# Kernel optimization log

Measured on AMD Instinct MI355X. Metric: run time of the kernel, lower is better.

Reference implementation:

```python
import jax, jax.numpy as jnp
import numpy as np

B, L, V, E, H = 64, 256, 256, 256, 1024

def setup_inputs() -> dict:
    key = jax.random.key(0)
    ks = jax.random.split(key, 7)
    inputs = jax.random.randint(ks[0], (B, L), 0, V, dtype=jnp.int32)
    embedding = jax.random.normal(ks[1], (V, E), dtype=jnp.float32)  # stddev=1.0 per emb_init
    # GRU weights: input projections (no bias) and hidden projections (with bias),
    # concatenated over gates [r, z, n].
    Wi = jax.random.normal(ks[2], (E, 3 * H), dtype=jnp.float32) / np.sqrt(E)
    Wh = jax.random.normal(ks[3], (H, 3 * H), dtype=jnp.float32) / np.sqrt(H)
    bh = jnp.zeros((3 * H,), dtype=jnp.float32)
    # Output dense (xavier_uniform-like scale)
    lim = np.sqrt(6.0 / (H + V))
    Wout = jax.random.uniform(ks[4], (H, V), dtype=jnp.float32, minval=-lim, maxval=lim)
    bout = jax.random.normal(ks[5], (V,), dtype=jnp.float32) * 1e-6
    return {"inputs": inputs, "embedding": embedding, "Wi": Wi, "Wh": Wh,
            "bh": bh, "Wout": Wout, "bout": bout}

def reference(inputs, embedding, Wi, Wh, bh, Wout, bout):
    # Embedding lookup: [B, L] -> [B, L, E]
    x = jnp.take(embedding, inputs, axis=0)
    # Precompute input-side gate projections for all timesteps (batched GEMM).
    xw = jnp.einsum('ble,ef->blf', x, Wi)  # [B, L, 3H]
    hidden = Wh.shape[0]

    def step(h, xw_t):
        gh = h @ Wh + bh                       # [B, 3H]
        xr, xz, xn = jnp.split(xw_t, 3, axis=-1)
        hr, hz, hn = jnp.split(gh, 3, axis=-1)
        r = jax.nn.sigmoid(xr + hr)
        z = jax.nn.sigmoid(xz + hz)
        n = jnp.tanh(xn + r * hn)
        h_new = (1.0 - z) * n + z * h          # GRUCell update
        return h_new, h_new

    h0 = jnp.zeros((x.shape[0], hidden), dtype=x.dtype)
    _, ys = jax.lax.scan(step, h0, jnp.swapaxes(xw, 0, 1))  # scan over time
    y = jnp.swapaxes(ys, 0, 1)                 # [B, L, H]
    logits = jnp.einsum('blh,hv->blv', y, Wout) + bout
    return logits
```

## Files before the change

kernel.cpp:

```cpp
#include <hip/hip_runtime.h>
#include <cstdint>
#include <math.h>

#define B_  64
#define L_  256
#define V_  256
#define E_  256
#define H_  1024
#define H3  3072

typedef __bf16 bf16x8 __attribute__((ext_vector_type(8)));
typedef float  f32x4  __attribute__((ext_vector_type(4)));

__device__ __forceinline__ unsigned short f2bf(float f) {
    union { float f; unsigned u; } v; v.f = f;
    unsigned r = v.u + 0x7fffu + ((v.u >> 16) & 1u);
    return (unsigned short)(r >> 16);
}

__device__ __forceinline__ int chunk_ok(bf16x8 v) {
    union { bf16x8 b; unsigned u[4]; } cv; cv.b = v;
    int ok = 1;
#pragma unroll
    for (int i = 0; i < 4; i++) {
        unsigned x = cv.u[i] ^ 0xAAAAAAAAu;
        ok &= (int)((x & 0xFFFFu) != 0u) & (int)((x >> 16) != 0u);
    }
    return ok;
}

__global__ __launch_bounds__(256) void prep_all(
        const float* __restrict__ Wh, const float* __restrict__ Wi,
        const float* __restrict__ Wout, const float* __restrict__ emb,
        unsigned short* __restrict__ WhT, unsigned short* __restrict__ WiT,
        unsigned short* __restrict__ WoutT, unsigned short* __restrict__ embB,
        unsigned short* __restrict__ h0b, uint4* __restrict__ poison) {
    __shared__ unsigned short tile[32][34];
    int bid = blockIdx.x;
    const float* src; unsigned short* dst; int rows, cols, nt, kt;
    if (bid < 3072)      { src = Wh;   dst = WhT;   rows = H_; cols = H3; nt = bid % 96; kt = bid / 96; }
    else if (bid < 3840) { int b = bid - 3072; src = Wi;   dst = WiT;   rows = E_; cols = H3; nt = b % 96; kt = b / 96; }
    else if (bid < 4096) { int b = bid - 3840; src = Wout; dst = WoutT; rows = H_; cols = V_; nt = b % 8;  kt = b / 8; }
    else if (bid < 4352) {
        int idx = (bid - 4096) * 256 + threadIdx.x;
        embB[idx] = f2bf(emb[idx]);
        h0b[idx]  = 0;
        return;
    } else {
        size_t T = (size_t)(bid - 4352) * 256 + threadIdx.x;
        uint4 v; v.x = v.y = v.z = v.w = 0xAAAAAAAAu;
        poison[T] = v;
        return;
    }
    int n0 = nt * 32, k0 = kt * 32;
    int tx = threadIdx.x & 31, ty = threadIdx.x >> 5;
#pragma unroll
    for (int j = 0; j < 32; j += 8)
        tile[tx][ty + j] = f2bf(src[(size_t)(k0 + ty + j) * cols + (n0 + tx)]);
    __syncthreads();
#pragma unroll
    for (int j = 0; j < 32; j += 8)
        dst[(size_t)(n0 + ty + j) * rows + (k0 + tx)] = tile[ty + j][tx];
}

__global__ __launch_bounds__(256, 1) void gru_persistent(
        unsigned short* __restrict__ hist,
        const unsigned short* __restrict__ WhT,
        const unsigned short* __restrict__ WiT,
        const unsigned short* __restrict__ embB,
        const int* __restrict__ tokens,
        const float* __restrict__ bh,
        unsigned short* __restrict__ yB) {
    __shared__ f32x4 red[2][4][6][64];

    int bid = blockIdx.x;
    int btile = bid & 3;
    int jtile = bid >> 2;
    int wave = threadIdx.x >> 6, lane = threadIdx.x & 63;
    int l16 = lane & 15, q = lane >> 4;
    int b0 = btile * 16, j0 = jtile * 16;
    int kbase = wave * 256;

    bf16x8 Wreg[3][8];
#pragma unroll
    for (int g = 0; g < 3; g++) {
        const bf16x8* Brow = (const bf16x8*)(WhT + (size_t)(g * H_ + j0 + l16) * H_);
#pragma unroll
        for (int kk = 0; kk < 8; kk++) {
            Wreg[g][kk] = Brow[(kbase >> 3) + kk * 4 + q];
            asm volatile("" : "+v"(Wreg[g][kk]));
        }
    }
    bf16x8 Wxreg[3][2];
#pragma unroll
    for (int g = 0; g < 3; g++) {
        const bf16x8* Bx = (const bf16x8*)(WiT + (size_t)(g * H_ + j0 + l16) * E_);
#pragma unroll
        for (int c = 0; c < 2; c++) {
            Wxreg[g][c] = Bx[wave * 8 + c * 4 + q];
            asm volatile("" : "+v"(Wxreg[g][c]));
        }
    }

    int Lp  = threadIdx.x & 63;
    int reg = threadIdx.x >> 6;
    int b_local = (Lp >> 4) * 4 + reg;
    int j_local = Lp & 15;
    int b = b0 + b_local, jg = j0 + j_local;
    float bhr = bh[jg];
    float bhz = bh[H_ + jg];
    float bhn = bh[2 * H_ + jg];
    asm volatile("" : "+v"(bhr), "+v"(bhz), "+v"(bhn));
    float hreg = 0.0f;

    const int tokrow = (b0 + l16) * L_;

    for (int t = 0; t < L_; t++) {
        const unsigned short* hist_t  = hist + (size_t)t * (B_ * H_);
        unsigned short*       hist_t1 = hist + (size_t)(t + 1) * (B_ * H_);

        int tok = tokens[tokrow + t];
        const bf16x8* Ax = (const bf16x8*)(embB + (size_t)tok * E_);
        bf16x8 ax0 = Ax[wave * 8 + q];
        bf16x8 ax1 = Ax[wave * 8 + 4 + q];
        f32x4 xacc[3] = {};
#pragma unroll
        for (int g = 0; g < 3; g++) {
            xacc[g] = __builtin_amdgcn_mfma_f32_16x16x32_bf16(ax0, Wxreg[g][0], xacc[g], 0, 0, 0);
            xacc[g] = __builtin_amdgcn_mfma_f32_16x16x32_bf16(ax1, Wxreg[g][1], xacc[g], 0, 0, 0);
        }

        const unsigned short* p = hist_t + (size_t)(b0 + l16) * H_ + kbase + q * 8;
        bf16x8 a0, a1, a2, a3, a4, a5, a6, a7;

        {
            int spins = 0;
            while (true) {
                asm volatile("global_load_dwordx4 %0, %1, off sc0 sc1" : "=v"(a0) : "v"(p));
                asm volatile("global_load_dwordx4 %0, %1, off sc0 sc1" : "=v"(a1) : "v"(p + 32));
                asm volatile("global_load_dwordx4 %0, %1, off sc0 sc1" : "=v"(a2) : "v"(p + 64));
                asm volatile("global_load_dwordx4 %0, %1, off sc0 sc1" : "=v"(a3) : "v"(p + 96));
                asm volatile("s_waitcnt vmcnt(0)"
                             : "+v"(a0), "+v"(a1), "+v"(a2), "+v"(a3) :: "memory");
                int ok = chunk_ok(a0) & chunk_ok(a1) & chunk_ok(a2) & chunk_ok(a3);
                if (__all(ok)) break;
                if (++spins > (1 << 18)) break;
                __builtin_amdgcn_s_sleep(1);
            }
        }
        asm volatile("global_load_dwordx4 %0, %1, off sc0 sc1" : "=v"(a4) : "v"(p + 128));
        asm volatile("global_load_dwordx4 %0, %1, off sc0 sc1" : "=v"(a5) : "v"(p + 160));
        asm volatile("global_load_dwordx4 %0, %1, off sc0 sc1" : "=v"(a6) : "v"(p + 192));
        asm volatile("global_load_dwordx4 %0, %1, off sc0 sc1" : "=v"(a7) : "v"(p + 224));

        f32x4 acc[3] = {};
#pragma unroll
        for (int g = 0; g < 3; g++) {
            acc[g] = __builtin_amdgcn_mfma_f32_16x16x32_bf16(a0, Wreg[g][0], acc[g], 0, 0, 0);
            acc[g] = __builtin_amdgcn_mfma_f32_16x16x32_bf16(a1, Wreg[g][1], acc[g], 0, 0, 0);
            acc[g] = __builtin_amdgcn_mfma_f32_16x16x32_bf16(a2, Wreg[g][2], acc[g], 0, 0, 0);
            acc[g] = __builtin_amdgcn_mfma_f32_16x16x32_bf16(a3, Wreg[g][3], acc[g], 0, 0, 0);
        }

        asm volatile("s_waitcnt vmcnt(0)"
                     : "+v"(a4), "+v"(a5), "+v"(a6), "+v"(a7) :: "memory");
        {
            int ok = chunk_ok(a4) & chunk_ok(a5) & chunk_ok(a6) & chunk_ok(a7);
            if (!__all(ok)) {
                int spins = 0;
                while (true) {
                    __builtin_amdgcn_s_sleep(1);
                    asm volatile("global_load_dwordx4 %0, %1, off sc0 sc1" : "=v"(a4) : "v"(p + 128));
                    asm volatile("global_load_dwordx4 %0, %1, off sc0 sc1" : "=v"(a5) : "v"(p + 160));
                    asm volatile("global_load_dwordx4 %0, %1, off sc0 sc1" : "=v"(a6) : "v"(p + 192));
                    asm volatile("global_load_dwordx4 %0, %1, off sc0 sc1" : "=v"(a7) : "v"(p + 224));
                    asm volatile("s_waitcnt vmcnt(0)"
                                 : "+v"(a4), "+v"(a5), "+v"(a6), "+v"(a7) :: "memory");
                    int ok2 = chunk_ok(a4) & chunk_ok(a5) & chunk_ok(a6) & chunk_ok(a7);
                    if (__all(ok2)) break;
                    if (++spins > (1 << 18)) break;
                }
            }
        }
#pragma unroll
        for (int g = 0; g < 3; g++) {
            acc[g] = __builtin_amdgcn_mfma_f32_16x16x32_bf16(a4, Wreg[g][4], acc[g], 0, 0, 0);
            acc[g] = __builtin_amdgcn_mfma_f32_16x16x32_bf16(a5, Wreg[g][5], acc[g], 0, 0, 0);
            acc[g] = __builtin_amdgcn_mfma_f32_16x16x32_bf16(a6, Wreg[g][6], acc[g], 0, 0, 0);
            acc[g] = __builtin_amdgcn_mfma_f32_16x16x32_bf16(a7, Wreg[g][7], acc[g], 0, 0, 0);
        }

        int par = t & 1;
#pragma unroll
        for (int g = 0; g < 3; g++) {
            red[par][wave][g][lane]     = acc[g];
            red[par][wave][3 + g][lane] = xacc[g];
        }
        __syncthreads();

        float gh0 = red[par][0][0][Lp][reg] + red[par][1][0][Lp][reg] + red[par][2][0][Lp][reg] + red[par][3][0][Lp][reg];
        float gh1 = red[par][0][1][Lp][reg] + red[par][1][1][Lp][reg] + red[par][2][1][Lp][reg] + red[par][3][1][Lp][reg];
        float gh2 = red[par][0][2][Lp][reg] + red[par][1][2][Lp][reg] + red[par][2][2][Lp][reg] + red[par][3][2][Lp][reg];
        float xr  = red[par][0][3][Lp][reg] + red[par][1][3][Lp][reg] + red[par][2][3][Lp][reg] + red[par][3][3][Lp][reg];
        float xz  = red[par][0][4][Lp][reg] + red[par][1][4][Lp][reg] + red[par][2][4][Lp][reg] + red[par][3][4][Lp][reg];
        float xn  = red[par][0][5][Lp][reg] + red[par][1][5][Lp][reg] + red[par][2][5][Lp][reg] + red[par][3][5][Lp][reg];

        float r = 1.0f / (1.0f + __expf(-(xr + gh0 + bhr)));
        float z = 1.0f / (1.0f + __expf(-(xz + gh1 + bhz)));
        float n = tanhf(xn + r * (gh2 + bhn));
        float hnew = (1.0f - z) * n + z * hreg;
        hreg = hnew;

        unsigned short hbv = f2bf(hnew);
        if (hbv == 0xAAAAu) hbv = 0xAAABu;

        {
            unsigned short* hp = hist_t1 + (size_t)b * H_ + jg;
            unsigned hv32 = hbv;
            asm volatile("global_store_short %0, %1, off sc0 sc1"
                         :: "v"(hp), "v"(hv32) : "memory");
        }
        yB[((size_t)b * L_ + t) * H_ + jg] = hbv;
    }
}

__global__ __launch_bounds__(256) void out_gemm(const unsigned short* __restrict__ yB,
                                                const unsigned short* __restrict__ WoutT,
                                                const float* __restrict__ bout,
                                                float* __restrict__ out) {
    int ntile = blockIdx.x;
    int mtile = blockIdx.y;
    int wave = threadIdx.x >> 6, lane = threadIdx.x & 63;
    int l16 = lane & 15, q = lane >> 4;

    int m = mtile * 64 + wave * 16 + l16;
    const bf16x8* Arow = (const bf16x8*)(yB + (size_t)m * H_);
    int n0 = ntile * 64;

    f32x4 acc[4] = {};
    for (int k0 = 0; k0 < H_; k0 += 32) {
        bf16x8 a = Arow[(k0 >> 3) + q];
#pragma unroll
        for (int j = 0; j < 4; j++) {
            const bf16x8* Brow = (const bf16x8*)(WoutT + (size_t)(n0 + j*16 + l16) * H_);
            bf16x8 b = Brow[(k0 >> 3) + q];
            acc[j] = __builtin_amdgcn_mfma_f32_16x16x32_bf16(a, b, acc[j], 0, 0, 0);
        }
    }
    int mrow = mtile * 64 + wave * 16 + q * 4;
#pragma unroll
    for (int j = 0; j < 4; j++) {
        int n = n0 + j * 16 + l16;
        float bias = bout[n];
#pragma unroll
        for (int r = 0; r < 4; r++)
            out[(size_t)(mrow + r) * V_ + n] = acc[j][r] + bias;
    }
}

extern "C" void kernel_launch(void* const* d_in, const int* in_sizes, int n_in,
                              void* d_out, int out_size, void* d_ws, size_t ws_size,
                              hipStream_t stream) {
    const int*   tokens = (const int*)  d_in[0];
    const float* emb    = (const float*)d_in[1];
    const float* Wi     = (const float*)d_in[2];
    const float* Wh     = (const float*)d_in[3];
    const float* bh     = (const float*)d_in[4];
    const float* Wout   = (const float*)d_in[5];
    const float* bout   = (const float*)d_in[6];
    float* out = (float*)d_out;

    char* ws = (char*)d_ws;
    size_t off = 0;
    auto alloc = [&](size_t bytes) -> void* {
        void* p = ws + off;
        off += (bytes + 255) & ~(size_t)255;
        return p;
    };
    unsigned short* WhT   = (unsigned short*)alloc((size_t)H3 * H_ * 2);
    unsigned short* WiT   = (unsigned short*)alloc((size_t)H3 * E_ * 2);
    unsigned short* WoutT = (unsigned short*)alloc((size_t)V_ * H_ * 2);
    unsigned short* embB  = (unsigned short*)alloc((size_t)V_ * E_ * 2);
    unsigned short* yB    = (unsigned short*)alloc((size_t)B_ * L_ * H_ * 2);
    unsigned short* hist  = (unsigned short*)alloc((size_t)(L_ + 1) * B_ * H_ * 2);

    prep_all<<<12544, 256, 0, stream>>>(Wh, Wi, Wout, emb, WhT, WiT, WoutT,
                                        embB, hist, (uint4*)(hist + (size_t)B_ * H_));

    {
        unsigned short* ah = hist;
        const unsigned short* aW = WhT; const unsigned short* aWx = WiT;
        const unsigned short* ae = embB; const int* at = tokens;
        const float* ab = bh; unsigned short* ay = yB;
        void* args[] = {&ah, &aW, &aWx, &ae, &at, &ab, &ay};
        hipError_t err = hipLaunchCooperativeKernel((void*)gru_persistent,
                                                    dim3(256), dim3(256), args, 0, stream);
        if (err != hipSuccess) {
            gru_persistent<<<dim3(256), dim3(256), 0, stream>>>(
                ah, aW, aWx, ae, at, ab, ay);
        }
    }

    out_gemm<<<dim3(4, 256), 256, 0, stream>>>(yB, WoutT, bout, out);
}
```

Baseline: 973.9 us.

## Give each GRU block two hidden tiles and relax coherent polling loads

Each persistent block now computes 32 hidden columns instead of 16, doubling the Wh/Wi weights held in registers. Only half of the launched blocks do work (g>=4 returns), so fewer blocks take part in each step's cross-block synchronisation. The polling loads of the previous hidden state start without the sc1 coherence bit and fall back to fully coherent loads with sleeps only after 512 spins. The gate nonlinearities switch to rcp-based sigmoid and tanh, and the LDS reduction layout is reorganised with an extra barrier. This risks register pressure from the doubled weight arrays and stale reads if the non-coherent polling misses fresh data.

```diff
diff --git a/kernel.cpp b/kernel.cpp
--- a/kernel.cpp
+++ b/kernel.cpp
@@ -27,6 +27,13 @@
         ok &= (int)((x & 0xFFFFu) != 0u) & (int)((x >> 16) != 0u);
     }
     return ok;
+}
+
+__device__ __forceinline__ float sigmoid_f(float x) {
+    return __builtin_amdgcn_rcpf(1.0f + __expf(-x));
+}
+__device__ __forceinline__ float tanh_f(float x) {
+    return 1.0f - 2.0f * __builtin_amdgcn_rcpf(1.0f + __expf(2.0f * x));
 }
 
 __global__ __launch_bounds__(256) void prep_all(
@@ -71,49 +78,61 @@
         const int* __restrict__ tokens,
         const float* __restrict__ bh,
         unsigned short* __restrict__ yB) {
-    __shared__ f32x4 red[2][4][6][64];
-
     int bid = blockIdx.x;
-    int btile = bid & 3;
-    int jtile = bid >> 2;
+    int g = bid & 7;
+    if (g >= 4) return;
+    int jpair = bid >> 3;
+    int b0 = g * 16;
+    int j0 = jpair * 32;
+
+    __shared__ float red[4][2][4][64][4];
+
     int wave = threadIdx.x >> 6, lane = threadIdx.x & 63;
     int l16 = lane & 15, q = lane >> 4;
-    int b0 = btile * 16, j0 = jtile * 16;
     int kbase = wave * 256;
 
-    bf16x8 Wreg[3][8];
-#pragma unroll
-    for (int g = 0; g < 3; g++) {
-        const bf16x8* Brow = (const bf16x8*)(WhT + (size_t)(g * H_ + j0 + l16) * H_);
-#pragma unroll
-        for (int kk = 0; kk < 8; kk++) {
-            Wreg[g][kk] = Brow[(kbase >> 3) + kk * 4 + q];
-            asm volatile("" : "+v"(Wreg[g][kk]));
-        }
-    }
-    bf16x8 Wxreg[3][2];
-#pragma unroll
-    for (int g = 0; g < 3; g++) {
-        const bf16x8* Bx = (const bf16x8*)(WiT + (size_t)(g * H_ + j0 + l16) * E_);
-#pragma unroll
-        for (int c = 0; c < 2; c++) {
-            Wxreg[g][c] = Bx[wave * 8 + c * 4 + q];
-            asm volatile("" : "+v"(Wxreg[g][c]));
-        }
-    }
-
-    int Lp  = threadIdx.x & 63;
-    int reg = threadIdx.x >> 6;
-    int b_local = (Lp >> 4) * 4 + reg;
-    int j_local = Lp & 15;
-    int b = b0 + b_local, jg = j0 + j_local;
-    float bhr = bh[jg];
-    float bhz = bh[H_ + jg];
-    float bhn = bh[2 * H_ + jg];
-    asm volatile("" : "+v"(bhr), "+v"(bhz), "+v"(bhn));
-    float hreg = 0.0f;
-
+    bf16x8 Wreg[2][3][8];
+#pragma unroll
+    for (int tl = 0; tl < 2; tl++) {
+#pragma unroll
+        for (int g3 = 0; g3 < 3; g3++) {
+            const bf16x8* Brow = (const bf16x8*)(WhT + (size_t)(g3 * H_ + j0 + tl * 16 + l16) * H_);
+#pragma unroll
+            for (int kk = 0; kk < 8; kk++) {
+                Wreg[tl][g3][kk] = Brow[(kbase >> 3) + kk * 4 + q];
+                asm volatile("" : "+v"(Wreg[tl][g3][kk]));
+            }
+        }
+    }
+    bf16x8 Wxreg[2][3][2];
+#pragma unroll
+    for (int tl = 0; tl < 2; tl++) {
+#pragma unroll
+        for (int g3 = 0; g3 < 3; g3++) {
+            const bf16x8* Bx = (const bf16x8*)(WiT + (size_t)(g3 * H_ + j0 + tl * 16 + l16) * E_);
+#pragma unroll
+            for (int c = 0; c < 2; c++) {
+                Wxreg[tl][g3][c] = Bx[wave * 8 + c * 4 + q];
+                asm volatile("" : "+v"(Wxreg[tl][g3][c]));
+            }
+        }
+    }
+
+    int j_local = lane & 15;
+    int b_local = (lane >> 4) * 4 + wave;
+    int b = b0 + b_local;
+    float bh_r[2], bh_z[2], bh_n[2];
+#pragma unroll
+    for (int tl = 0; tl < 2; tl++) {
+        int jg = j0 + tl * 16 + j_local;
+        bh_r[tl] = bh[jg];
+        bh_z[tl] = bh[H_ + jg];
+        bh_n[tl] = bh[2 * H_ + jg];
+        asm volatile("" : "+v"(bh_r[tl]), "+v"(bh_z[tl]), "+v"(bh_n[tl]));
+    }
+    float hreg[2] = {0.0f, 0.0f};
     const int tokrow = (b0 + l16) * L_;
+    int coh = 0;
 
     for (int t = 0; t < L_; t++) {
         const unsigned short* hist_t  = hist + (size_t)t * (B_ * H_);
@@ -123,11 +142,15 @@
         const bf16x8* Ax = (const bf16x8*)(embB + (size_t)tok * E_);
         bf16x8 ax0 = Ax[wave * 8 + q];
         bf16x8 ax1 = Ax[wave * 8 + 4 + q];
-        f32x4 xacc[3] = {};
-#pragma unroll
-        for (int g = 0; g < 3; g++) {
-            xacc[g] = __builtin_amdgcn_mfma_f32_16x16x32_bf16(ax0, Wxreg[g][0], xacc[g], 0, 0, 0);
-            xacc[g] = __builtin_amdgcn_mfma_f32_16x16x32_bf16(ax1, Wxreg[g][1], xacc[g], 0, 0, 0);
+        f32x4 accr[2] = {}, accz[2] = {}, acchn[2] = {}, accxn[2] = {};
+#pragma unroll
+        for (int tl = 0; tl < 2; tl++) {
+            accr[tl]  = __builtin_amdgcn_mfma_f32_16x16x32_bf16(ax0, Wxreg[tl][0][0], accr[tl], 0, 0, 0);
+            accr[tl]  = __builtin_amdgcn_mfma_f32_16x16x32_bf16(ax1, Wxreg[tl][0][1], accr[tl], 0, 0, 0);
+            accz[tl]  = __builtin_amdgcn_mfma_f32_16x16x32_bf16(ax0, Wxreg[tl][1][0], accz[tl], 0, 0, 0);
+            accz[tl]  = __builtin_amdgcn_mfma_f32_16x16x32_bf16(ax1, Wxreg[tl][1][1], accz[tl], 0, 0, 0);
+            accxn[tl] = __builtin_amdgcn_mfma_f32_16x16x32_bf16(ax0, Wxreg[tl][2][0], accxn[tl], 0, 0, 0);
+            accxn[tl] = __builtin_amdgcn_mfma_f32_16x16x32_bf16(ax1, Wxreg[tl][2][1], accxn[tl], 0, 0, 0);
         }
 
         const unsigned short* p = hist_t + (size_t)(b0 + l16) * H_ + kbase + q * 8;
@@ -136,30 +159,53 @@
         {
             int spins = 0;
             while (true) {
-                asm volatile("global_load_dwordx4 %0, %1, off sc0 sc1" : "=v"(a0) : "v"(p));
-                asm volatile("global_load_dwordx4 %0, %1, off sc0 sc1" : "=v"(a1) : "v"(p + 32));
-                asm volatile("global_load_dwordx4 %0, %1, off sc0 sc1" : "=v"(a2) : "v"(p + 64));
-                asm volatile("global_load_dwordx4 %0, %1, off sc0 sc1" : "=v"(a3) : "v"(p + 96));
+                if (coh) {
+                    asm volatile("global_load_dwordx4 %0, %1, off sc0 sc1" : "=v"(a0) : "v"(p));
+                    asm volatile("global_load_dwordx4 %0, %1, off sc0 sc1" : "=v"(a1) : "v"(p + 32));
+                    asm volatile("global_load_dwordx4 %0, %1, off sc0 sc1" : "=v"(a2) : "v"(p + 64));
+                    asm volatile("global_load_dwordx4 %0, %1, off sc0 sc1" : "=v"(a3) : "v"(p + 96));
+                } else {
+                    asm volatile("global_load_dwordx4 %0, %1, off sc0" : "=v"(a0) : "v"(p));
+                    asm volatile("global_load_dwordx4 %0, %1, off sc0" : "=v"(a1) : "v"(p + 32));
+                    asm volatile("global_load_dwordx4 %0, %1, off sc0" : "=v"(a2) : "v"(p + 64));
+                    asm volatile("global_load_dwordx4 %0, %1, off sc0" : "=v"(a3) : "v"(p + 96));
+                }
                 asm volatile("s_waitcnt vmcnt(0)"
                              : "+v"(a0), "+v"(a1), "+v"(a2), "+v"(a3) :: "memory");
                 int ok = chunk_ok(a0) & chunk_ok(a1) & chunk_ok(a2) & chunk_ok(a3);
                 if (__all(ok)) break;
-                if (++spins > (1 << 18)) break;
-                __builtin_amdgcn_s_sleep(1);
-            }
-        }
-        asm volatile("global_load_dwordx4 %0, %1, off sc0 sc1" : "=v"(a4) : "v"(p + 128));
-        asm volatile("global_load_dwordx4 %0, %1, off sc0 sc1" : "=v"(a5) : "v"(p + 160));
-        asm volatile("global_load_dwordx4 %0, %1, off sc0 sc1" : "=v"(a6) : "v"(p + 192));
-        asm volatile("global_load_dwordx4 %0, %1, off sc0 sc1" : "=v"(a7) : "v"(p + 224));
-
-        f32x4 acc[3] = {};
-#pragma unroll
-        for (int g = 0; g < 3; g++) {
-            acc[g] = __builtin_amdgcn_mfma_f32_16x16x32_bf16(a0, Wreg[g][0], acc[g], 0, 0, 0);
-            acc[g] = __builtin_amdgcn_mfma_f32_16x16x32_bf16(a1, Wreg[g][1], acc[g], 0, 0, 0);
-            acc[g] = __builtin_amdgcn_mfma_f32_16x16x32_bf16(a2, Wreg[g][2], acc[g], 0, 0, 0);
-            acc[g] = __builtin_amdgcn_mfma_f32_16x16x32_bf16(a3, Wreg[g][3], acc[g], 0, 0, 0);
+                ++spins;
+                if (spins == 512) coh = 1;
+                if (spins > (1 << 18)) break;
+                if (coh) __builtin_amdgcn_s_sleep(1);
+            }
+        }
+        if (coh) {
+            asm volatile("global_load_dwordx4 %0, %1, off sc0 sc1" : "=v"(a4) : "v"(p + 128));
+            asm volatile("global_load_dwordx4 %0, %1, off sc0 sc1" : "=v"(a5) : "v"(p + 160));
+            asm volatile("global_load_dwordx4 %0, %1, off sc0 sc1" : "=v"(a6) : "v"(p + 192));
+            asm volatile("global_load_dwordx4 %0, %1, off sc0 sc1" : "=v"(a7) : "v"(p + 224));
+        } else {
+            asm volatile("global_load_dwordx4 %0, %1, off sc0" : "=v"(a4) : "v"(p + 128));
+            asm volatile("global_load_dwordx4 %0, %1, off sc0" : "=v"(a5) : "v"(p + 160));
+            asm volatile("global_load_dwordx4 %0, %1, off sc0" : "=v"(a6) : "v"(p + 192));
+            asm volatile("global_load_dwordx4 %0, %1, off sc0" : "=v"(a7) : "v"(p + 224));
+        }
+
+#pragma unroll
+        for (int tl = 0; tl < 2; tl++) {
+            accr[tl]  = __builtin_amdgcn_mfma_f32_16x16x32_bf16(a0, Wreg[tl][0][0], accr[tl], 0, 0, 0);
+            accr[tl]  = __builtin_amdgcn_mfma_f32_16x16x32_bf16(a1, Wreg[tl][0][1], accr[tl], 0, 0, 0);
+            accr[tl]  = __builtin_amdgcn_mfma_f32_16x16x32_bf16(a2, Wreg[tl][0][2], accr[tl], 0, 0, 0);
+            accr[tl]  = __builtin_amdgcn_mfma_f32_16x16x32_bf16(a3, Wreg[tl][0][3], accr[tl], 0, 0, 0);
+            accz[tl]  = __builtin_amdgcn_mfma_f32_16x16x32_bf16(a0, Wreg[tl][1][0], accz[tl], 0, 0, 0);
+            accz[tl]  = __builtin_amdgcn_mfma_f32_16x16x32_bf16(a1, Wreg[tl][1][1], accz[tl], 0, 0, 0);
+            accz[tl]  = __builtin_amdgcn_mfma_f32_16x16x32_bf16(a2, Wreg[tl][1][2], accz[tl], 0, 0, 0);
+            accz[tl]  = __builtin_amdgcn_mfma_f32_16x16x32_bf16(a3, Wreg[tl][1][3], accz[tl], 0, 0, 0);
+            acchn[tl] = __builtin_amdgcn_mfma_f32_16x16x32_bf16(a0, Wreg[tl][2][0], acchn[tl], 0, 0, 0);
+            acchn[tl] = __builtin_amdgcn_mfma_f32_16x16x32_bf16(a1, Wreg[tl][2][1], acchn[tl], 0, 0, 0);
+            acchn[tl] = __builtin_amdgcn_mfma_f32_16x16x32_bf16(a2, Wreg[tl][2][2], acchn[tl], 0, 0, 0);
+            acchn[tl] = __builtin_amdgcn_mfma_f32_16x16x32_bf16(a3, Wreg[tl][2][3], acchn[tl], 0, 0, 0);
         }
 
         asm volatile("s_waitcnt vmcnt(0)"
@@ -169,58 +215,82 @@
             if (!__all(ok)) {
                 int spins = 0;
                 while (true) {
-                    __builtin_amdgcn_s_sleep(1);
-                    asm volatile("global_load_dwordx4 %0, %1, off sc0 sc1" : "=v"(a4) : "v"(p + 128));
-                    asm volatile("global_load_dwordx4 %0, %1, off sc0 sc1" : "=v"(a5) : "v"(p + 160));
-                    asm volatile("global_load_dwordx4 %0, %1, off sc0 sc1" : "=v"(a6) : "v"(p + 192));
-                    asm volatile("global_load_dwordx4 %0, %1, off sc0 sc1" : "=v"(a7) : "v"(p + 224));
+                    if (coh) {
+                        asm volatile("global_load_dwordx4 %0, %1, off sc0 sc1" : "=v"(a4) : "v"(p + 128));
+                        asm volatile("global_load_dwordx4 %0, %1, off sc0 sc1" : "=v"(a5) : "v"(p + 160));
+                        asm volatile("global_load_dwordx4 %0, %1, off sc0 sc1" : "=v"(a6) : "v"(p + 192));
+                        asm volatile("global_load_dwordx4 %0, %1, off sc0 sc1" : "=v"(a7) : "v"(p + 224));
+                    } else {
+                        asm volatile("global_load_dwordx4 %0, %1, off sc0" : "=v"(a4) : "v"(p + 128));
+                        asm volatile("global_load_dwordx4 %0, %1, off sc0" : "=v"(a5) : "v"(p + 160));
+                        asm volatile("global_load_dwordx4 %0, %1, off sc0" : "=v"(a6) : "v"(p + 192));
+                        asm volatile("global_load_dwordx4 %0, %1, off sc0" : "=v"(a7) : "v"(p + 224));
+                    }
                     asm volatile("s_waitcnt vmcnt(0)"
                                  : "+v"(a4), "+v"(a5), "+v"(a6), "+v"(a7) :: "memory");
                     int ok2 = chunk_ok(a4) & chunk_ok(a5) & chunk_ok(a6) & chunk_ok(a7);
                     if (__all(ok2)) break;
-                    if (++spins > (1 << 18)) break;
+                    ++spins;
+                    if (spins == 512) coh = 1;
+                    if (spins > (1 << 18)) break;
+                    if (coh) __builtin_amdgcn_s_sleep(1);
                 }
             }
         }
 #pragma unroll
-        for (int g = 0; g < 3; g++) {
-            acc[g] = __builtin_amdgcn_mfma_f32_16x16x32_bf16(a4, Wreg[g][4], acc[g], 0, 0, 0);
-            acc[g] = __builtin_amdgcn_mfma_f32_16x16x32_bf16(a5, Wreg[g][5], acc[g], 0, 0, 0);
-            acc[g] = __builtin_amdgcn_mfma_f32_16x16x32_bf16(a6, Wreg[g][6], acc[g], 0, 0, 0);
-            acc[g] = __builtin_amdgcn_mfma_f32_16x16x32_bf16(a7, Wreg[g][7], acc[g], 0, 0, 0);
-        }
-
-        int par = t & 1;
-#pragma unroll
-        for (int g = 0; g < 3; g++) {
-            red[par][wave][g][lane]     = acc[g];
-            red[par][wave][3 + g][lane] = xacc[g];
-        }
+        for (int tl = 0; tl < 2; tl++) {
+            accr[tl]  = __builtin_amdgcn_mfma_f32_16x16x32_bf16(a4, Wreg[tl][0][4], accr[tl], 0, 0, 0);
+            accr[tl]  = __builtin_amdgcn_mfma_f32_16x16x32_bf16(a5, Wreg[tl][0][5], accr[tl], 0, 0, 0);
+            accr[tl]  = __builtin_amdgcn_mfma_f32_16x16x32_bf16(a6, Wreg[tl][0][6], accr[tl], 0, 0, 0);
+            accr[tl]  = __builtin_amdgcn_mfma_f32_16x16x32_bf16(a7, Wreg[tl][0][7], accr[tl], 0, 0, 0);
+            accz[tl]  = __builtin_amdgcn_mfma_f32_16x16x32_bf16(a4, Wreg[tl][1][4], accz[tl], 0, 0, 0);
+            accz[tl]  = __builtin_amdgcn_mfma_f32_16x16x32_bf16(a5, Wreg[tl][1][5], accz[tl], 0, 0, 0);
+            accz[tl]  = __builtin_amdgcn_mfma_f32_16x16x32_bf16(a6, Wreg[tl][1][6], accz[tl], 0, 0, 0);
+            accz[tl]  = __builtin_amdgcn_mfma_f32_16x16x32_bf16(a7, Wreg[tl][1][7], accz[tl], 0, 0, 0);
+            acchn[tl] = __builtin_amdgcn_mfma_f32_16x16x32_bf16(a4, Wreg[tl][2][4], acchn[tl], 0, 0, 0);
+            acchn[tl] = __builtin_amdgcn_mfma_f32_16x16x32_bf16(a5, Wreg[tl][2][5], acchn[tl], 0, 0, 0);
+            acchn[tl] = __builtin_amdgcn_mfma_f32_16x16x32_bf16(a6, Wreg[tl][2][6], acchn[tl], 0, 0, 0);
+            acchn[tl] = __builtin_amdgcn_mfma_f32_16x16x32_bf16(a7, Wreg[tl][2][7], acchn[tl], 0, 0, 0);
+        }
+
         __syncthreads();
-
-        float gh0 = red[par][0][0][Lp][reg] + red[par][1][0][Lp][reg] + red[par][2][0][Lp][reg] + red[par][3][0][Lp][reg];
-        float gh1 = red[par][0][1][Lp][reg] + red[par][1][1][Lp][reg] + red[par][2][1][Lp][reg] + red[par][3][1][Lp][reg];
-        float gh2 = red[par][0][2][Lp][reg] + red[par][1][2][Lp][reg] + red[par][2][2][Lp][reg] + red[par][3][2][Lp][reg];
-        float xr  = red[par][0][3][Lp][reg] + red[par][1][3][Lp][reg] + red[par][2][3][Lp][reg] + red[par][3][3][Lp][reg];
-        float xz  = red[par][0][4][Lp][reg] + red[par][1][4][Lp][reg] + red[par][2][4][Lp][reg] + red[par][3][4][Lp][reg];
-        float xn  = red[par][0][5][Lp][reg] + red[par][1][5][Lp][reg] + red[par][2][5][Lp][reg] + red[par][3][5][Lp][reg];
-
-        float r = 1.0f / (1.0f + __expf(-(xr + gh0 + bhr)));
-        float z = 1.0f / (1.0f + __expf(-(xz + gh1 + bhz)));
-        float n = tanhf(xn + r * (gh2 + bhn));
-        float hnew = (1.0f - z) * n + z * hreg;
-        hreg = hnew;
-
-        unsigned short hbv = f2bf(hnew);
-        if (hbv == 0xAAAAu) hbv = 0xAAABu;
-
-        {
+#pragma unroll
+        for (int tl = 0; tl < 2; tl++) {
+            *(f32x4*)&red[wave][tl][0][lane][0] = accr[tl];
+            *(f32x4*)&red[wave][tl][1][lane][0] = accz[tl];
+            *(f32x4*)&red[wave][tl][2][lane][0] = acchn[tl];
+            *(f32x4*)&red[wave][tl][3][lane][0] = accxn[tl];
+        }
+        __syncthreads();
+
+#pragma unroll
+        for (int tl = 0; tl < 2; tl++) {
+            float s0 = 0.f, s1 = 0.f, s2 = 0.f, s3 = 0.f;
+#pragma unroll
+            for (int w = 0; w < 4; w++) {
+                s0 += red[w][tl][0][lane][wave];
+                s1 += red[w][tl][1][lane][wave];
+                s2 += red[w][tl][2][lane][wave];
+                s3 += red[w][tl][3][lane][wave];
+            }
+            float r = sigmoid_f(s0 + bh_r[tl]);
+            float z = sigmoid_f(s1 + bh_z[tl]);
+            float n = tanh_f(s3 + r * (s2 + bh_n[tl]));
+            float hnew = (1.0f - z) * n + z * hreg[tl];
+            hreg[tl] = hnew;
+
+            unsigned short hbv = f2bf(hnew);
+            if (hbv == 0xAAAAu) hbv = 0xAAABu;
+
+            int jg = j0 + tl * 16 + j_local;
             unsigned short* hp = hist_t1 + (size_t)b * H_ + jg;
             unsigned hv32 = hbv;
             asm volatile("global_store_short %0, %1, off sc0 sc1"
                          :: "v"(hp), "v"(hv32) : "memory");
-        }
-        yB[((size_t)b * L_ + t) * H_ + jg] = hbv;
+            asm volatile("global_store_short %0, %1, off"
+                         :: "v"(hp), "v"(hv32) : "memory");
+            yB[((size_t)b * L_ + t) * H_ + jg] = hbv;
+        }
     }
 }
 
```

Result: slower. 1.529 ms (+57.0%).

## Coalesce GRU hidden-state stores via LDS and single-pass poll on all chunks

Applied to the files above, without the earlier changes.

Each block now stages its 16x16 new hidden-state tile in shared memory. A few lanes then write it as 16-byte stores to both the history buffer and yB, replacing many 2-byte stores. The readiness poll issues all eight chunk loads up front and waits once. Because chunks are now written atomically in 16-byte units, it checks only the head word of each chunk, and it sleeps only after 16 spins. The next timestep's token and embedding row are prefetched during the current step. In exchange there is an extra block barrier per step, and correctness depends on the 16-byte stores being seen whole.

```diff
diff --git a/kernel.cpp b/kernel.cpp
--- a/kernel.cpp
+++ b/kernel.cpp
@@ -11,6 +11,7 @@
 
 typedef __bf16 bf16x8 __attribute__((ext_vector_type(8)));
 typedef float  f32x4  __attribute__((ext_vector_type(4)));
+typedef unsigned u32x4 __attribute__((ext_vector_type(4)));
 
 __device__ __forceinline__ unsigned short f2bf(float f) {
     union { float f; unsigned u; } v; v.f = f;
@@ -18,15 +19,10 @@
     return (unsigned short)(r >> 16);
 }
 
-__device__ __forceinline__ int chunk_ok(bf16x8 v) {
+__device__ __forceinline__ int head_ok(bf16x8 v) {
     union { bf16x8 b; unsigned u[4]; } cv; cv.b = v;
-    int ok = 1;
-#pragma unroll
-    for (int i = 0; i < 4; i++) {
-        unsigned x = cv.u[i] ^ 0xAAAAAAAAu;
-        ok &= (int)((x & 0xFFFFu) != 0u) & (int)((x >> 16) != 0u);
-    }
-    return ok;
+    unsigned x = cv.u[0];
+    return (int)((x & 0xFFFFu) != 0xAAAAu) & (int)((x >> 16) != 0xAAAAu);
 }
 
 __global__ __launch_bounds__(256) void prep_all(
@@ -72,6 +68,7 @@
         const float* __restrict__ bh,
         unsigned short* __restrict__ yB) {
     __shared__ f32x4 red[2][4][6][64];
+    __shared__ unsigned short htile[16][24];
 
     int bid = blockIdx.x;
     int btile = bid & 3;
@@ -106,52 +103,74 @@
     int reg = threadIdx.x >> 6;
     int b_local = (Lp >> 4) * 4 + reg;
     int j_local = Lp & 15;
-    int b = b0 + b_local, jg = j0 + j_local;
-    float bhr = bh[jg];
-    float bhz = bh[H_ + jg];
-    float bhn = bh[2 * H_ + jg];
+    float bhr = bh[j0 + j_local];
+    float bhz = bh[H_ + j0 + j_local];
+    float bhn = bh[2 * H_ + j0 + j_local];
     asm volatile("" : "+v"(bhr), "+v"(bhz), "+v"(bhn));
     float hreg = 0.0f;
 
     const int tokrow = (b0 + l16) * L_;
+    int srow  = wave * 4 + ((lane >> 1) & 3);
+    int shalf = lane & 1;
+
+    int tok = tokens[tokrow];
+    const bf16x8* Ax0p = (const bf16x8*)(embB + (size_t)tok * E_);
+    bf16x8 ax0 = Ax0p[wave * 8 + q];
+    bf16x8 ax1 = Ax0p[wave * 8 + 4 + q];
 
     for (int t = 0; t < L_; t++) {
         const unsigned short* hist_t  = hist + (size_t)t * (B_ * H_);
         unsigned short*       hist_t1 = hist + (size_t)(t + 1) * (B_ * H_);
-
-        int tok = tokens[tokrow + t];
-        const bf16x8* Ax = (const bf16x8*)(embB + (size_t)tok * E_);
-        bf16x8 ax0 = Ax[wave * 8 + q];
-        bf16x8 ax1 = Ax[wave * 8 + 4 + q];
+        const unsigned short* p = hist_t + (size_t)(b0 + l16) * H_ + kbase + q * 8;
+
+        bf16x8 a0, a1, a2, a3, a4, a5, a6, a7;
+        asm volatile("global_load_dwordx4 %0, %1, off sc0 sc1" : "=v"(a0) : "v"(p));
+        asm volatile("global_load_dwordx4 %0, %1, off sc0 sc1" : "=v"(a1) : "v"(p + 32));
+        asm volatile("global_load_dwordx4 %0, %1, off sc0 sc1" : "=v"(a2) : "v"(p + 64));
+        asm volatile("global_load_dwordx4 %0, %1, off sc0 sc1" : "=v"(a3) : "v"(p + 96));
+        asm volatile("global_load_dwordx4 %0, %1, off sc0 sc1" : "=v"(a4) : "v"(p + 128));
+        asm volatile("global_load_dwordx4 %0, %1, off sc0 sc1" : "=v"(a5) : "v"(p + 160));
+        asm volatile("global_load_dwordx4 %0, %1, off sc0 sc1" : "=v"(a6) : "v"(p + 192));
+        asm volatile("global_load_dwordx4 %0, %1, off sc0 sc1" : "=v"(a7) : "v"(p + 224));
+
         f32x4 xacc[3] = {};
 #pragma unroll
         for (int g = 0; g < 3; g++) {
             xacc[g] = __builtin_amdgcn_mfma_f32_16x16x32_bf16(ax0, Wxreg[g][0], xacc[g], 0, 0, 0);
             xacc[g] = __builtin_amdgcn_mfma_f32_16x16x32_bf16(ax1, Wxreg[g][1], xacc[g], 0, 0, 0);
         }
-
-        const unsigned short* p = hist_t + (size_t)(b0 + l16) * H_ + kbase + q * 8;
-        bf16x8 a0, a1, a2, a3, a4, a5, a6, a7;
+        int tnext = (t + 1 < L_) ? (t + 1) : (L_ - 1);
+        const int* tp = tokens + tokrow + tnext;
+        int tok_next;
+        asm volatile("global_load_dword %0, %1, off" : "=v"(tok_next) : "v"(tp));
 
         {
             int spins = 0;
             while (true) {
+                asm volatile("s_waitcnt vmcnt(0)"
+                             : "+v"(a0), "+v"(a1), "+v"(a2), "+v"(a3),
+                               "+v"(a4), "+v"(a5), "+v"(a6), "+v"(a7), "+v"(tok_next)
+                             :: "memory");
+                int ok = head_ok(a0) & head_ok(a1) & head_ok(a2) & head_ok(a3)
+                       & head_ok(a4) & head_ok(a5) & head_ok(a6) & head_ok(a7);
+                if (__all(ok)) break;
+                if (++spins > (1 << 18)) break;
+                if (spins > 16) __builtin_amdgcn_s_sleep(1);
                 asm volatile("global_load_dwordx4 %0, %1, off sc0 sc1" : "=v"(a0) : "v"(p));
                 asm volatile("global_load_dwordx4 %0, %1, off sc0 sc1" : "=v"(a1) : "v"(p + 32));
                 asm volatile("global_load_dwordx4 %0, %1, off sc0 sc1" : "=v"(a2) : "v"(p + 64));
                 asm volatile("global_load_dwordx4 %0, %1, off sc0 sc1" : "=v"(a3) : "v"(p + 96));
-                asm volatile("s_waitcnt vmcnt(0)"
-                             : "+v"(a0), "+v"(a1), "+v"(a2), "+v"(a3) :: "memory");
-                int ok = chunk_ok(a0) & chunk_ok(a1) & chunk_ok(a2) & chunk_ok(a3);
-                if (__all(ok)) break;
-                if (++spins > (1 << 18)) break;
-                __builtin_amdgcn_s_sleep(1);
+                asm volatile("global_load_dwordx4 %0, %1, off sc0 sc1" : "=v"(a4) : "v"(p + 128));
+                asm volatile("global_load_dwordx4 %0, %1, off sc0 sc1" : "=v"(a5) : "v"(p + 160));
+                asm volatile("global_load_dwordx4 %0, %1, off sc0 sc1" : "=v"(a6) : "v"(p + 192));
+                asm volatile("global_load_dwordx4 %0, %1, off sc0 sc1" : "=v"(a7) : "v"(p + 224));
             }
         }
-        asm volatile("global_load_dwordx4 %0, %1, off sc0 sc1" : "=v"(a4) : "v"(p + 128));
-        asm volatile("global_load_dwordx4 %0, %1, off sc0 sc1" : "=v"(a5) : "v"(p + 160));
-        asm volatile("global_load_dwordx4 %0, %1, off sc0 sc1" : "=v"(a6) : "v"(p + 192));
-        asm volatile("global_load_dwordx4 %0, %1, off sc0 sc1" : "=v"(a7) : "v"(p + 224));
+
+        const bf16x8* Axn = (const bf16x8*)(embB + (size_t)tok_next * E_);
+        bf16x8 ax0n, ax1n;
+        asm volatile("global_load_dwordx4 %0, %1, off" : "=v"(ax0n) : "v"(Axn + wave * 8 + q));
+        asm volatile("global_load_dwordx4 %0, %1, off" : "=v"(ax1n) : "v"(Axn + wave * 8 + 4 + q));
 
         f32x4 acc[3] = {};
 #pragma unroll
@@ -160,30 +179,6 @@
             acc[g] = __builtin_amdgcn_mfma_f32_16x16x32_bf16(a1, Wreg[g][1], acc[g], 0, 0, 0);
             acc[g] = __builtin_amdgcn_mfma_f32_16x16x32_bf16(a2, Wreg[g][2], acc[g], 0, 0, 0);
             acc[g] = __builtin_amdgcn_mfma_f32_16x16x32_bf16(a3, Wreg[g][3], acc[g], 0, 0, 0);
-        }
-
-        asm volatile("s_waitcnt vmcnt(0)"
-                     : "+v"(a4), "+v"(a5), "+v"(a6), "+v"(a7) :: "memory");
-        {
-            int ok = chunk_ok(a4) & chunk_ok(a5) & chunk_ok(a6) & chunk_ok(a7);
-            if (!__all(ok)) {
-                int spins = 0;
-                while (true) {
-                    __builtin_amdgcn_s_sleep(1);
-                    asm volatile("global_load_dwordx4 %0, %1, off sc0 sc1" : "=v"(a4) : "v"(p + 128));
-                    asm volatile("global_load_dwordx4 %0, %1, off sc0 sc1" : "=v"(a5) : "v"(p + 160));
-                    asm volatile("global_load_dwordx4 %0, %1, off sc0 sc1" : "=v"(a6) : "v"(p + 192));
-                    asm volatile("global_load_dwordx4 %0, %1, off sc0 sc1" : "=v"(a7) : "v"(p + 224));
-                    asm volatile("s_waitcnt vmcnt(0)"
-                                 : "+v"(a4), "+v"(a5), "+v"(a6), "+v"(a7) :: "memory");
-                    int ok2 = chunk_ok(a4) & chunk_ok(a5) & chunk_ok(a6) & chunk_ok(a7);
-                    if (__all(ok2)) break;
-                    if (++spins > (1 << 18)) break;
-                }
-            }
-        }
-#pragma unroll
-        for (int g = 0; g < 3; g++) {
             acc[g] = __builtin_amdgcn_mfma_f32_16x16x32_bf16(a4, Wreg[g][4], acc[g], 0, 0, 0);
             acc[g] = __builtin_amdgcn_mfma_f32_16x16x32_bf16(a5, Wreg[g][5], acc[g], 0, 0, 0);
             acc[g] = __builtin_amdgcn_mfma_f32_16x16x32_bf16(a6, Wreg[g][6], acc[g], 0, 0, 0);
@@ -214,13 +209,20 @@
         unsigned short hbv = f2bf(hnew);
         if (hbv == 0xAAAAu) hbv = 0xAAABu;
 
-        {
-            unsigned short* hp = hist_t1 + (size_t)b * H_ + jg;
-            unsigned hv32 = hbv;
-            asm volatile("global_store_short %0, %1, off sc0 sc1"
-                         :: "v"(hp), "v"(hv32) : "memory");
-        }
-        yB[((size_t)b * L_ + t) * H_ + jg] = hbv;
+        asm volatile("s_waitcnt vmcnt(0)" : "+v"(ax0n), "+v"(ax1n) :: "memory");
+
+        htile[b_local][j_local] = hbv;
+        __syncthreads();
+        if (lane < 8) {
+            u32x4 hv4 = *(const u32x4*)&htile[srow][shalf * 8];
+            unsigned short* hp = hist_t1 + (size_t)(b0 + srow) * H_ + j0 + shalf * 8;
+            asm volatile("global_store_dwordx4 %0, %1, off sc0 sc1"
+                         :: "v"(hp), "v"(hv4) : "memory");
+            unsigned short* yp = yB + ((size_t)(b0 + srow) * L_ + t) * H_ + j0 + shalf * 8;
+            asm volatile("global_store_dwordx4 %0, %1, off"
+                         :: "v"(yp), "v"(hv4) : "memory");
+        }
+        ax0 = ax0n; ax1 = ax1n;
     }
 }
 
```

Result: slower. 1.091 ms (+12.1%).
